# Performance work log

Measured on AMD Instinct MI355X. Metric: run time of the kernel, lower is better.

## Reference

```python
import jax, jax.numpy as jnp
import numpy as np


def setup_inputs() -> dict:
    key = jax.random.key(0)
    ks = jax.random.split(key, 7)
    B, S, D, H = 8, 1024, 1024, 16
    dk = D // H
    return {
        "q": jax.random.normal(ks[0], (B, S, D), dtype=jnp.float32),
        "k": jax.random.normal(ks[1], (B, S, D), dtype=jnp.float32),
        "v": jax.random.normal(ks[2], (B, S, D), dtype=jnp.float32),
        "Wq": jax.random.normal(ks[3], (H, dk, D), dtype=jnp.float32) * 0.03,
        "Wk": jax.random.normal(ks[4], (H, dk, D), dtype=jnp.float32) * 0.03,
        "Wv": jax.random.normal(ks[5], (dk, D), dtype=jnp.float32) * 0.03,
        "Wo": jax.random.normal(ks[6], (D, dk), dtype=jnp.float32) * 0.03,
    }


def reference(q, k, v, Wq, Wk, Wv, Wo):
    # per-head projections (Linear weight layout [out, in]); shared V projection
    dk = Wq.shape[1]
    qs = jnp.einsum("bsd,hed->bhse", q, Wq)          # [B,H,S,dk]
    ks_ = jnp.einsum("btd,hed->bhte", k, Wk)         # [B,H,S,dk]
    vs = jnp.einsum("btd,ed->bte", v, Wv)            # [B,S,dk] shared across heads
    scale = jnp.sqrt(jnp.asarray(dk, dtype=qs.dtype))
    scores = jnp.einsum("bhse,bhte->bhst", qs, ks_) / scale
    attn = jax.nn.softmax(scores, axis=-1)           # [B,H,Sq,Sk]
    heads = jnp.einsum("bhst,bte->bhse", attn, vs)   # [B,H,S,dk]
    head_mean = jnp.mean(heads, axis=1)              # mean over heads -> [B,S,dk]
    outputs = jnp.einsum("bse,de->bsd", head_mean, Wo)
    attn_out = jnp.transpose(attn, (0, 2, 1, 3))     # stacked at dim=2: [B,Sq,H,Sk]
    return outputs, attn_out
```

## Files before the change

kernel.cpp:

```cpp
#include <hip/hip_runtime.h>
#include <hip/hip_bf16.h>


typedef __attribute__((ext_vector_type(4))) float f32x4;
typedef __attribute__((ext_vector_type(8))) short bf16x8;
typedef __attribute__((ext_vector_type(2))) unsigned int uint2v;

#define MFMA16(a, b, c) __builtin_amdgcn_mfma_f32_16x16x32_bf16((a), (b), (c), 0, 0, 0)

__device__ __forceinline__ unsigned int rne16(float f) {
  unsigned int u = __float_as_uint(f);
  return u + 0x7fffu + ((u >> 16) & 1u);
}
__device__ __forceinline__ unsigned int pack2bf(float a, float b) {
  return (rne16(a) >> 16) | (rne16(b) & 0xffff0000u);
}
__device__ __forceinline__ short f2bf(float f) {
  return (short)(rne16(f) >> 16);
}
__device__ __forceinline__ float bf2f(short s) {
  return __uint_as_float(((unsigned int)(unsigned short)s) << 16);
}

__global__ __launch_bounds__(256) void proj_qk_kernel(
    const float* __restrict__ qin, const float* __restrict__ kin,
    const float* __restrict__ Wq, const float* __restrict__ Wk,
    __hip_bfloat16* __restrict__ qs, __hip_bfloat16* __restrict__ ks)
{
  const int K = 1024, N = 1024;
  __shared__ short a_lds[128][40];
  __shared__ short b_lds[128][40];
  const int tid  = threadIdx.x;
  const int lane = tid & 63, wid = tid >> 6;
  const int g = lane >> 4, r = lane & 15;
  const bool isK = blockIdx.y >= 8;
  const float* A = isK ? kin : qin;
  const float* W = isK ? Wk : Wq;
  __hip_bfloat16* C = isK ? ks : qs;
  const float scale = isK ? 1.0f : 0.125f;
  const int m0 = blockIdx.x * 128;
  const int n0 = (blockIdx.y & 7) * 128;
  const int wm = (wid >> 1) * 64, wn = (wid & 1) * 64;
  const int lrow = tid >> 3, lcol = (tid & 7) * 4;

  f32x4 acc[4][4];
#pragma unroll
  for (int i = 0; i < 4; ++i)
#pragma unroll
    for (int j = 0; j < 4; ++j) acc[i][j] = (f32x4){0.f, 0.f, 0.f, 0.f};

  for (int k0 = 0; k0 < K; k0 += 32) {
    float4 av[4], wv[4];
#pragma unroll
    for (int p = 0; p < 4; ++p) {
      av[p] = *(const float4*)&A[(m0 + lrow + p * 32) * K + k0 + lcol];
      wv[p] = *(const float4*)&W[(n0 + lrow + p * 32) * K + k0 + lcol];
    }
    __syncthreads();
#pragma unroll
    for (int p = 0; p < 4; ++p) {
      uint2v ua = {pack2bf(av[p].x, av[p].y), pack2bf(av[p].z, av[p].w)};
      uint2v uw = {pack2bf(wv[p].x, wv[p].y), pack2bf(wv[p].z, wv[p].w)};
      *(uint2v*)&a_lds[lrow + p * 32][lcol] = ua;
      *(uint2v*)&b_lds[lrow + p * 32][lcol] = uw;
    }
    __syncthreads();
    bf16x8 af[4], bf[4];
#pragma unroll
    for (int t = 0; t < 4; ++t) {
      af[t] = *(bf16x8*)&a_lds[wm + t * 16 + r][g * 8];
      bf[t] = *(bf16x8*)&b_lds[wn + t * 16 + r][g * 8];
    }
#pragma unroll
    for (int mt = 0; mt < 4; ++mt)
#pragma unroll
      for (int nt = 0; nt < 4; ++nt)
        acc[mt][nt] = MFMA16(af[mt], bf[nt], acc[mt][nt]);
  }

#pragma unroll
  for (int mt = 0; mt < 4; ++mt)
#pragma unroll
    for (int nt = 0; nt < 4; ++nt) {
      const int n = n0 + wn + nt * 16 + r;
#pragma unroll
      for (int j = 0; j < 4; ++j) {
        const int m = m0 + wm + mt * 16 + 4 * g + j;
        C[m * N + n] = __float2bfloat16(acc[mt][nt][j] * scale);
      }
    }
}

__global__ __launch_bounds__(256) void proj_v_kernel(
    const float* __restrict__ vin, const float* __restrict__ Wv,
    __hip_bfloat16* __restrict__ vsT)
{
  const int K = 1024;
  __shared__ short a_lds[128][40];
  __shared__ short b_lds[64][40];
  const int tid  = threadIdx.x;
  const int lane = tid & 63, wid = tid >> 6;
  const int g = lane >> 4, r = lane & 15;
  const int m0 = blockIdx.x * 128;
  const int wm = wid * 32;
  const int lrow = tid >> 3, lcol = (tid & 7) * 4;

  f32x4 acc[2][4];
#pragma unroll
  for (int i = 0; i < 2; ++i)
#pragma unroll
    for (int j = 0; j < 4; ++j) acc[i][j] = (f32x4){0.f, 0.f, 0.f, 0.f};

  for (int k0 = 0; k0 < K; k0 += 32) {
    float4 av[4], wv2[2];
#pragma unroll
    for (int p = 0; p < 4; ++p)
      av[p] = *(const float4*)&vin[(m0 + lrow + p * 32) * K + k0 + lcol];
#pragma unroll
    for (int p = 0; p < 2; ++p)
      wv2[p] = *(const float4*)&Wv[(lrow + p * 32) * K + k0 + lcol];
    __syncthreads();
#pragma unroll
    for (int p = 0; p < 4; ++p) {
      uint2v ua = {pack2bf(av[p].x, av[p].y), pack2bf(av[p].z, av[p].w)};
      *(uint2v*)&a_lds[lrow + p * 32][lcol] = ua;
    }
#pragma unroll
    for (int p = 0; p < 2; ++p) {
      uint2v uw = {pack2bf(wv2[p].x, wv2[p].y), pack2bf(wv2[p].z, wv2[p].w)};
      *(uint2v*)&b_lds[lrow + p * 32][lcol] = uw;
    }
    __syncthreads();
    bf16x8 af[2], bf[4];
#pragma unroll
    for (int t = 0; t < 2; ++t) af[t] = *(bf16x8*)&a_lds[wm + t * 16 + r][g * 8];
#pragma unroll
    for (int t = 0; t < 4; ++t) bf[t] = *(bf16x8*)&b_lds[t * 16 + r][g * 8];
#pragma unroll
    for (int mt = 0; mt < 2; ++mt)
#pragma unroll
      for (int nt = 0; nt < 4; ++nt)
        acc[mt][nt] = MFMA16(af[mt], bf[nt], acc[mt][nt]);
  }

#pragma unroll
  for (int mt = 0; mt < 2; ++mt)
#pragma unroll
    for (int nt = 0; nt < 4; ++nt) {
      const int e = nt * 16 + r;
#pragma unroll
      for (int j = 0; j < 4; ++j) {
        const int m = m0 + wm + mt * 16 + 4 * g + j;
        const int b = m >> 10, t = m & 1023;
        vsT[b * 65536 + e * 1024 + t] = __float2bfloat16(acc[mt][nt][j]);
      }
    }
}

__global__ __launch_bounds__(256) void attn_kernel(
    const __hip_bfloat16* __restrict__ qs_, const __hip_bfloat16* __restrict__ ks_,
    const __hip_bfloat16* __restrict__ vsT_, float* __restrict__ attn_out,
    __hip_bfloat16* __restrict__ heads_)
{
  const int S = 1024, H = 16;
  const int tid = threadIdx.x, lane = tid & 63, wid = tid >> 6;
  const int g = lane >> 4, r = lane & 15;
  const int qb = blockIdx.x, h = blockIdx.y, b = blockIdx.z;
  const int bh = b * H + h;
  const int qrow = qb * 64 + wid * 16;
  __shared__ short p_lds[4][16][40];

  const short* qsp = (const short*)qs_;
  const short* ksp = (const short*)ks_;
  const short* vsp = (const short*)vsT_;
  short* headsp = (short*)heads_;

  const int qidx = (b * S + qrow + r) * 1024 + h * 64;
  const bf16x8 qf0 = *(const bf16x8*)&qsp[qidx + g * 8];
  const bf16x8 qf1 = *(const bf16x8*)&qsp[qidx + 32 + g * 8];
  const int kbase = (b * S + r) * 1024 + h * 64 + g * 8;

  float ls0 = 0.f, ls1 = 0.f, ls2 = 0.f, ls3 = 0.f;
  for (int t0 = 0; t0 < S; t0 += 64) {
    bf16x8 kf[8];
#pragma unroll
    for (int u = 0; u < 4; ++u) {
      kf[2 * u]     = *(const bf16x8*)&ksp[kbase + (t0 + 16 * u) * 1024];
      kf[2 * u + 1] = *(const bf16x8*)&ksp[kbase + (t0 + 16 * u) * 1024 + 32];
    }
    float lp[4];
#pragma unroll
    for (int u = 0; u < 4; ++u) {
      f32x4 s = (f32x4){0.f, 0.f, 0.f, 0.f};
      s = MFMA16(kf[2 * u], qf0, s);
      s = MFMA16(kf[2 * u + 1], qf1, s);
      lp[u] = (__expf(s[0]) + __expf(s[1])) + (__expf(s[2]) + __expf(s[3]));
    }
    ls0 += lp[0]; ls1 += lp[1]; ls2 += lp[2]; ls3 += lp[3];
  }
  float ls = (ls0 + ls1) + (ls2 + ls3);
  ls += __shfl_xor(ls, 16);
  ls += __shfl_xor(ls, 32);
  const float inv = 1.f / ls;

  f32x4 hacc[4];
#pragma unroll
  for (int i = 0; i < 4; ++i) hacc[i] = (f32x4){0.f, 0.f, 0.f, 0.f};

  const int arow = ((b * S + qrow + r) * H + h) * S;
  const int vbase = b * 65536 + r * 1024 + g * 8;

  for (int tc = 0; tc < S; tc += 32) {
    bf16x8 vf[4], kf[4];
#pragma unroll
    for (int nt = 0; nt < 4; ++nt)
      vf[nt] = *(const bf16x8*)&vsp[vbase + nt * 16384 + tc];
#pragma unroll
    for (int sub = 0; sub < 2; ++sub) {
      kf[2 * sub]     = *(const bf16x8*)&ksp[kbase + (tc + 16 * sub) * 1024];
      kf[2 * sub + 1] = *(const bf16x8*)&ksp[kbase + (tc + 16 * sub) * 1024 + 32];
    }
#pragma unroll
    for (int sub = 0; sub < 2; ++sub) {
      f32x4 s = (f32x4){0.f, 0.f, 0.f, 0.f};
      s = MFMA16(kf[2 * sub], qf0, s);
      s = MFMA16(kf[2 * sub + 1], qf1, s);
      f32x4 p;
      p[0] = __expf(s[0]) * inv;
      p[1] = __expf(s[1]) * inv;
      p[2] = __expf(s[2]) * inv;
      p[3] = __expf(s[3]) * inv;
      __builtin_nontemporal_store(p, (f32x4*)&attn_out[arow + tc + sub * 16 + 4 * g]);
      uint2v pk = {pack2bf(p[0], p[1]), pack2bf(p[2], p[3])};
      *(uint2v*)&p_lds[wid][r][sub * 16 + 4 * g] = pk;
    }
    asm volatile("s_waitcnt lgkmcnt(0)" ::: "memory");
    const bf16x8 pa = *(bf16x8*)&p_lds[wid][r][g * 8];
#pragma unroll
    for (int nt = 0; nt < 4; ++nt)
      hacc[nt] = MFMA16(pa, vf[nt], hacc[nt]);
  }

#pragma unroll
  for (int nt = 0; nt < 4; ++nt)
#pragma unroll
    for (int j = 0; j < 4; ++j)
      headsp[(bh * S + qrow + 4 * g + j) * 64 + nt * 16 + r] =
          f2bf(hacc[nt][j]);
}

__global__ __launch_bounds__(256) void out_kernel(
    const __hip_bfloat16* __restrict__ heads_, const float* __restrict__ Wo,
    float* __restrict__ out)
{
  __shared__ float hm[16][64];
  const int tid = threadIdx.x;
  const int m0 = blockIdx.x * 16;
  const short* headsp = (const short*)heads_;

  {
    const int row = tid >> 4, e4 = (tid & 15) * 4;
    const int m = m0 + row, b = m >> 10, s = m & 1023;
    float a0 = 0.f, a1 = 0.f, a2 = 0.f, a3 = 0.f;
    for (int hh = 0; hh < 16; ++hh) {
      typedef __attribute__((ext_vector_type(4))) short short4v;
      const short4v hv =
          *(const short4v*)&headsp[((b * 16 + hh) * 1024 + s) * 64 + e4];
      a0 += bf2f(hv[0]); a1 += bf2f(hv[1]); a2 += bf2f(hv[2]); a3 += bf2f(hv[3]);
    }
    const float sc = 1.f / 16.f;
    hm[row][e4 + 0] = a0 * sc; hm[row][e4 + 1] = a1 * sc;
    hm[row][e4 + 2] = a2 * sc; hm[row][e4 + 3] = a3 * sc;
  }
  __syncthreads();

  for (int c = 0; c < 4; ++c) {
    const int d = c * 256 + tid;
    float4 wo4[16];
#pragma unroll
    for (int i = 0; i < 16; ++i) wo4[i] = *(const float4*)&Wo[d * 64 + i * 4];
    for (int row = 0; row < 16; ++row) {
      float a = 0.f;
#pragma unroll
      for (int i = 0; i < 16; ++i) {
        const float4 h4 = *(const float4*)&hm[row][i * 4];
        a += h4.x * wo4[i].x + h4.y * wo4[i].y + h4.z * wo4[i].z + h4.w * wo4[i].w;
      }
      out[(m0 + row) * 1024 + d] = a;
    }
  }
}

extern "C" void kernel_launch(void* const* d_in, const int* in_sizes, int n_in,
                              void* d_out, int out_size, void* d_ws, size_t ws_size,
                              hipStream_t stream) {
  const float* q  = (const float*)d_in[0];
  const float* k  = (const float*)d_in[1];
  const float* v  = (const float*)d_in[2];
  const float* Wq = (const float*)d_in[3];
  const float* Wk = (const float*)d_in[4];
  const float* Wv = (const float*)d_in[5];
  const float* Wo = (const float*)d_in[6];

  float* out0 = (float*)d_out;
  float* attn = out0 + (size_t)8 * 1024 * 1024;

  char* ws = (char*)d_ws;
  __hip_bfloat16* qs    = (__hip_bfloat16*)(ws);
  __hip_bfloat16* ksbuf = (__hip_bfloat16*)(ws + (16u << 20));
  __hip_bfloat16* vsT   = (__hip_bfloat16*)(ws + (32u << 20));
  __hip_bfloat16* heads = (__hip_bfloat16*)(ws + (33u << 20));

  dim3 blk(256);
  proj_qk_kernel<<<dim3(64, 16), blk, 0, stream>>>(q, k, Wq, Wk, qs, ksbuf);
  proj_v_kernel<<<dim3(64), blk, 0, stream>>>(v, Wv, vsT);
  attn_kernel<<<dim3(16, 16, 8), blk, 0, stream>>>(qs, ksbuf, vsT, attn, heads);
  out_kernel<<<dim3(512), blk, 0, stream>>>(heads, Wo, out0);
}
```

Before: 503.8 us.

## Cache unnormalized bf16 exp scores in registers to skip second QK pass

The attention kernel now keeps the unnormalized exponentials from the first pass as packed bf16 in a 128-entry register array. The second pass reuses them instead of reloading K and recomputing the MFMAs and exps. Normalization is moved to the end of the PV accumulation by scaling with a per-row inverse obtained through a shuffle, and launch bounds now request 2 blocks per CU. The cost is heavy register pressure, with possible spilling or lower occupancy. The attention probabilities written out are also now rounded through bf16 rather than computed in fp32, which lowers output precision.

```diff
diff --git a/kernel.cpp b/kernel.cpp
--- a/kernel.cpp
+++ b/kernel.cpp
@@ -20,6 +20,12 @@
 }
 __device__ __forceinline__ float bf2f(short s) {
   return __uint_as_float(((unsigned int)(unsigned short)s) << 16);
+}
+__device__ __forceinline__ float bflo(unsigned int u) {
+  return __uint_as_float(u << 16);
+}
+__device__ __forceinline__ float bfhi(unsigned int u) {
+  return __uint_as_float(u & 0xffff0000u);
 }
 
 __global__ __launch_bounds__(256) void proj_qk_kernel(
@@ -157,7 +163,7 @@
     }
 }
 
-__global__ __launch_bounds__(256) void attn_kernel(
+__global__ __launch_bounds__(256, 2) void attn_kernel(
     const __hip_bfloat16* __restrict__ qs_, const __hip_bfloat16* __restrict__ ks_,
     const __hip_bfloat16* __restrict__ vsT_, float* __restrict__ attn_out,
     __hip_bfloat16* __restrict__ heads_)
@@ -180,28 +186,38 @@
   const bf16x8 qf1 = *(const bf16x8*)&qsp[qidx + 32 + g * 8];
   const int kbase = (b * S + r) * 1024 + h * 64 + g * 8;
 
-  float ls0 = 0.f, ls1 = 0.f, ls2 = 0.f, ls3 = 0.f;
-  for (int t0 = 0; t0 < S; t0 += 64) {
+  unsigned int pk[128];
+  float lsa0 = 0.f, lsa1 = 0.f, lsa2 = 0.f, lsa3 = 0.f;
+#pragma unroll
+  for (int i = 0; i < 16; ++i) {
+    const int t0 = i * 64;
     bf16x8 kf[8];
 #pragma unroll
     for (int u = 0; u < 4; ++u) {
       kf[2 * u]     = *(const bf16x8*)&ksp[kbase + (t0 + 16 * u) * 1024];
       kf[2 * u + 1] = *(const bf16x8*)&ksp[kbase + (t0 + 16 * u) * 1024 + 32];
     }
-    float lp[4];
+    float es[4];
 #pragma unroll
     for (int u = 0; u < 4; ++u) {
       f32x4 s = (f32x4){0.f, 0.f, 0.f, 0.f};
       s = MFMA16(kf[2 * u], qf0, s);
       s = MFMA16(kf[2 * u + 1], qf1, s);
-      lp[u] = (__expf(s[0]) + __expf(s[1])) + (__expf(s[2]) + __expf(s[3]));
-    }
-    ls0 += lp[0]; ls1 += lp[1]; ls2 += lp[2]; ls3 += lp[3];
-  }
-  float ls = (ls0 + ls1) + (ls2 + ls3);
+      const float e0 = __expf(s[0]), e1 = __expf(s[1]);
+      const float e2 = __expf(s[2]), e3 = __expf(s[3]);
+      pk[i * 8 + 2 * u]     = pack2bf(e0, e1);
+      pk[i * 8 + 2 * u + 1] = pack2bf(e2, e3);
+      es[u] = (e0 + e1) + (e2 + e3);
+    }
+    lsa0 += es[0]; lsa1 += es[1]; lsa2 += es[2]; lsa3 += es[3];
+  }
+  float ls = (lsa0 + lsa1) + (lsa2 + lsa3);
   ls += __shfl_xor(ls, 16);
   ls += __shfl_xor(ls, 32);
   const float inv = 1.f / ls;
+  float invq[4];
+#pragma unroll
+  for (int j = 0; j < 4; ++j) invq[j] = __shfl(inv, 4 * g + j);
 
   f32x4 hacc[4];
 #pragma unroll
@@ -210,30 +226,24 @@
   const int arow = ((b * S + qrow + r) * H + h) * S;
   const int vbase = b * 65536 + r * 1024 + g * 8;
 
-  for (int tc = 0; tc < S; tc += 32) {
-    bf16x8 vf[4], kf[4];
+#pragma unroll
+  for (int j = 0; j < 32; ++j) {
+    const int tc = j * 32;
+    bf16x8 vf[4];
 #pragma unroll
     for (int nt = 0; nt < 4; ++nt)
       vf[nt] = *(const bf16x8*)&vsp[vbase + nt * 16384 + tc];
-#pragma unroll
-    for (int sub = 0; sub < 2; ++sub) {
-      kf[2 * sub]     = *(const bf16x8*)&ksp[kbase + (tc + 16 * sub) * 1024];
-      kf[2 * sub + 1] = *(const bf16x8*)&ksp[kbase + (tc + 16 * sub) * 1024 + 32];
-    }
-#pragma unroll
-    for (int sub = 0; sub < 2; ++sub) {
-      f32x4 s = (f32x4){0.f, 0.f, 0.f, 0.f};
-      s = MFMA16(kf[2 * sub], qf0, s);
-      s = MFMA16(kf[2 * sub + 1], qf1, s);
-      f32x4 p;
-      p[0] = __expf(s[0]) * inv;
-      p[1] = __expf(s[1]) * inv;
-      p[2] = __expf(s[2]) * inv;
-      p[3] = __expf(s[3]) * inv;
-      __builtin_nontemporal_store(p, (f32x4*)&attn_out[arow + tc + sub * 16 + 4 * g]);
-      uint2v pk = {pack2bf(p[0], p[1]), pack2bf(p[2], p[3])};
-      *(uint2v*)&p_lds[wid][r][sub * 16 + 4 * g] = pk;
-    }
+    uint2v w0 = {pk[4 * j + 0], pk[4 * j + 1]};
+    uint2v w1 = {pk[4 * j + 2], pk[4 * j + 3]};
+    *(uint2v*)&p_lds[wid][r][0 * 16 + 4 * g] = w0;
+    *(uint2v*)&p_lds[wid][r][1 * 16 + 4 * g] = w1;
+    f32x4 p0, p1;
+    p0[0] = bflo(pk[4 * j + 0]) * inv; p0[1] = bfhi(pk[4 * j + 0]) * inv;
+    p0[2] = bflo(pk[4 * j + 1]) * inv; p0[3] = bfhi(pk[4 * j + 1]) * inv;
+    p1[0] = bflo(pk[4 * j + 2]) * inv; p1[1] = bfhi(pk[4 * j + 2]) * inv;
+    p1[2] = bflo(pk[4 * j + 3]) * inv; p1[3] = bfhi(pk[4 * j + 3]) * inv;
+    __builtin_nontemporal_store(p0, (f32x4*)&attn_out[arow + tc + 4 * g]);
+    __builtin_nontemporal_store(p1, (f32x4*)&attn_out[arow + tc + 16 + 4 * g]);
     asm volatile("s_waitcnt lgkmcnt(0)" ::: "memory");
     const bf16x8 pa = *(bf16x8*)&p_lds[wid][r][g * 8];
 #pragma unroll
@@ -246,7 +256,7 @@
 #pragma unroll
     for (int j = 0; j < 4; ++j)
       headsp[(bh * S + qrow + 4 * g + j) * 64 + nt * 16 + r] =
-          f2bf(hacc[nt][j]);
+          f2bf(hacc[nt][j] * invq[j]);
 }
 
 __global__ __launch_bounds__(256) void out_kernel(
```

Result: slower. 560.7 us (+11.3%).
